# Optimization experiments

Hardware: AMD Instinct MI355X
Metric: run time of the kernel (lower is better)

Reference implementation:

```python
import jax, jax.numpy as jnp
import numpy as np

N_NODES = 50000
N_EDGES = 800000
IN_DIM = 128
HIDDEN = 256
N_CLASSES = 16
N_GRAPHS = 128


def setup_inputs() -> dict:
    key = jax.random.key(0)
    ks = jax.random.split(key, 10)
    x = jax.random.normal(ks[0], (N_NODES, IN_DIM), dtype=jnp.float32)
    edge_index = jax.random.randint(ks[1], (2, N_EDGES), 0, N_NODES, dtype=jnp.int64)
    batch = jnp.sort(jax.random.randint(ks[2], (N_NODES,), 0, N_GRAPHS, dtype=jnp.int64))
    s = 1.0 / np.sqrt(HIDDEN)
    return {
        "x": x,
        "edge_index": edge_index,
        "batch": batch,
        "W_in": jax.random.normal(ks[3], (IN_DIM, HIDDEN), dtype=jnp.float32) / np.sqrt(IN_DIM),
        "b_in": jnp.zeros((HIDDEN,), dtype=jnp.float32),
        "W1": jax.random.normal(ks[4], (HIDDEN, HIDDEN), dtype=jnp.float32) * s,
        "b1": jnp.zeros((HIDDEN,), dtype=jnp.float32),
        "W2": jax.random.normal(ks[5], (HIDDEN, HIDDEN), dtype=jnp.float32) * s,
        "b2": jnp.zeros((HIDDEN,), dtype=jnp.float32),
        "W_out": jax.random.normal(ks[6], (HIDDEN, N_CLASSES), dtype=jnp.float32) * s,
        "b_out": jnp.zeros((N_CLASSES,), dtype=jnp.float32),
    }


def gcn_conv(x, W, b, src, dst):
    # PyG GCNConv: add self-loops, symmetric norm D^-1/2 A D^-1/2, scatter-add at target.
    h = x @ W  # [N, H]
    n = x.shape[0]
    # degree of target nodes, including one self-loop per node
    deg = jax.ops.segment_sum(jnp.ones_like(dst, dtype=h.dtype), dst, num_segments=n) + 1.0
    dinv = deg ** -0.5  # [N]
    norm = dinv[src] * dinv[dst]  # [E]
    msg = h[src] * norm[:, None]  # [E, H]  gather + scale
    agg = jax.ops.segment_sum(msg, dst, num_segments=n)  # scatter-add
    agg = agg + h * (dinv * dinv)[:, None]  # self-loop contribution
    return agg + b


def reference(x, edge_index, batch, W_in, b_in, W1, b1, W2, b2, W_out, b_out):
    src, dst = edge_index[0], edge_index[1]
    h = x @ W_in + b_in
    # layer 1 (dropout is identity in eval mode)
    h = jax.nn.relu(gcn_conv(h, W1, b1, src, dst))
    # layer 2
    h = jax.nn.relu(gcn_conv(h, W2, b2, src, dst))
    # global mean pool over graphs
    sums = jax.ops.segment_sum(h, batch, num_segments=N_GRAPHS)  # [G, H]
    counts = jax.ops.segment_sum(jnp.ones((h.shape[0],), h.dtype), batch, num_segments=N_GRAPHS)
    pooled = sums / jnp.maximum(counts, 1.0)[:, None]
    return pooled @ W_out + b_out  # [G, n_classes]
```

## Files before the change

kernel.cpp:

```cpp
#include <hip/hip_runtime.h>
#include <hip/hip_bf16.h>

typedef __attribute__((ext_vector_type(8))) short bf16x8;
typedef __attribute__((ext_vector_type(4))) float f32x4;

__device__ __forceinline__ unsigned short f2bf(float f) {
    unsigned u = __float_as_uint(f);
    u += 0x7fff + ((u >> 16) & 1);
    return (unsigned short)(u >> 16);
}
__device__ __forceinline__ float bf2f(unsigned short s) {
    return __uint_as_float(((unsigned)s) << 16);
}

#define GL2LDS16(g, l) __builtin_amdgcn_global_load_lds(                      \
        (const __attribute__((address_space(1))) void*)(g),                   \
        (__attribute__((address_space(3))) void*)(l), 16, 0, 0)


__global__ __launch_bounds__(256) void fused_misc_kernel(
        const float* __restrict__ W2, unsigned short* __restrict__ Wt2,
        const float* __restrict__ x, unsigned short* __restrict__ xb, int n4,
        const float* __restrict__ W_in, const float* __restrict__ b_in,
        const float* __restrict__ W1,
        unsigned short* __restrict__ WfT, float* __restrict__ bv,
        const int* __restrict__ src, const int* __restrict__ dst,
        int* __restrict__ cursor, unsigned short* __restrict__ csr16,
        unsigned short* __restrict__ zrow,
        float* __restrict__ sums, int* __restrict__ counts,
        int e, int FB, int WB) {
    __shared__ float row[256];
    __shared__ unsigned short tile[64][65];
    int b = blockIdx.x;
    if (b < FB) {
        int i = b * 256 + threadIdx.x;
        if (i < e) {
            int d = dst[i];
            int p = atomicAdd(&cursor[d], 1);
            if (p < 64) csr16[((size_t)d << 6) + p] = (unsigned short)src[i];
        }
    } else if (b < FB + WB) {
        int k = b - FB;
        int nn = threadIdx.x;
        row[nn] = (k < 128) ? W_in[k * 256 + nn] : b_in[nn];
        __syncthreads();
        float acc = 0.f;
        #pragma unroll 4
        for (int j = 0; j < 256; ++j) acc = fmaf(row[j], W1[j * 256 + nn], acc);
        if (k < 128) WfT[(size_t)nn * 128 + k] = f2bf(acc);
        else bv[nn] = acc;
    } else if (b < FB + WB + 16) {
        int t = b - FB - WB;
        int ti = t >> 2, tj = t & 3;
        int rq = threadIdx.x >> 4;
        int c0 = (threadIdx.x & 15) * 4;
        #pragma unroll
        for (int rr = 0; rr < 64; rr += 16) {
            int r = rr + rq;
            float4 v = *(const float4*)&W2[(size_t)(ti * 64 + r) * 256 + tj * 64 + c0];
            tile[r][c0]     = f2bf(v.x);
            tile[r][c0 + 1] = f2bf(v.y);
            tile[r][c0 + 2] = f2bf(v.z);
            tile[r][c0 + 3] = f2bf(v.w);
        }
        __syncthreads();
        #pragma unroll
        for (int rr = 0; rr < 64; rr += 16) {
            int nrow = rr + rq;
            ushort4 o;
            o.x = tile[c0][nrow];
            o.y = tile[c0 + 1][nrow];
            o.z = tile[c0 + 2][nrow];
            o.w = tile[c0 + 3][nrow];
            *(ushort4*)&Wt2[(size_t)(tj * 64 + nrow) * 256 + ti * 64 + c0] = o;
        }
    } else if (b == FB + WB + 16) {
        if (threadIdx.x < 128) ((unsigned*)zrow)[threadIdx.x] = 0u;
    } else if (b < FB + WB + 16 + 1 + 129) {
        int j = b - (FB + WB + 17);
        if (j < 128) sums[j * 256 + threadIdx.x] = 0.f;
        else if (threadIdx.x < 128) counts[threadIdx.x] = 0;
    } else {
        int i = (b - FB - WB - 17 - 129) * 256 + threadIdx.x;
        if (i < n4) {
            float4 v = ((const float4*)x)[i];
            ushort4 o;
            o.x = f2bf(v.x); o.y = f2bf(v.y); o.z = f2bf(v.z); o.w = f2bf(v.w);
            ((ushort4*)xb)[i] = o;
        }
    }
}


template <int MODE>
__global__ __launch_bounds__(256) void gemm_bf16(const unsigned short* __restrict__ A,
                                                 const unsigned short* __restrict__ Wt,
                                                 const float* __restrict__ aux,
                                                 const float* __restrict__ aux2,
                                                 const float* __restrict__ aux3,
                                                 unsigned short* __restrict__ C,
                                                 int M, int K) {
    __shared__ unsigned short As[128 * 64];
    __shared__ unsigned short Bs[128 * 64];
    const int tid  = threadIdx.x;
    const int lane = tid & 63;
    const int w    = tid >> 6;
    const int wr   = w >> 1, wc = w & 1;
    const int row0 = blockIdx.x * 128;
    const int col0 = blockIdx.y * 128;
    const int mlane = lane & 15, quad = lane >> 4;

    f32x4 acc[4][4];
    #pragma unroll
    for (int i = 0; i < 4; ++i)
        #pragma unroll
        for (int j = 0; j < 4; ++j) acc[i][j] = f32x4{0.f, 0.f, 0.f, 0.f};

    const unsigned short* gA[4]; const unsigned short* gB[4];
    unsigned short* lA[4]; unsigned short* lB[4];
    #pragma unroll
    for (int p = 0; p < 4; ++p) {
        int cid = (p * 4 + w) * 64 + lane;
        int row = cid >> 3, slot = cid & 7;
        int rowA = row0 + row; if (rowA >= M) rowA = M - 1;
        gA[p] = A + (size_t)rowA * K + slot * 8;
        gB[p] = Wt + (size_t)(col0 + row) * K + slot * 8;
        lA[p] = &As[((p * 4 + w) * 64) * 8];
        lB[p] = &Bs[((p * 4 + w) * 64) * 8];
    }

    for (int k0 = 0; k0 < K; k0 += 64) {
        #pragma unroll
        for (int p = 0; p < 4; ++p) GL2LDS16(gA[p] + k0, lA[p]);
        #pragma unroll
        for (int p = 0; p < 4; ++p) GL2LDS16(gB[p] + k0, lB[p]);
        __syncthreads();
        #pragma unroll
        for (int ks = 0; ks < 2; ++ks) {
            bf16x8 af[4], bfv[4];
            #pragma unroll
            for (int i = 0; i < 4; ++i)
                af[i] = *(const bf16x8*)&As[(wr * 64 + i * 16 + mlane) * 64 + ks * 32 + quad * 8];
            #pragma unroll
            for (int j = 0; j < 4; ++j)
                bfv[j] = *(const bf16x8*)&Bs[(wc * 64 + j * 16 + mlane) * 64 + ks * 32 + quad * 8];
            #pragma unroll
            for (int i = 0; i < 4; ++i)
                #pragma unroll
                for (int j = 0; j < 4; ++j)
                    acc[i][j] = __builtin_amdgcn_mfma_f32_16x16x32_bf16(af[i], bfv[j], acc[i][j], 0, 0, 0);
        }
        __syncthreads();
    }

    float bj[4], cj[4];
    if (MODE == 0) {
        #pragma unroll
        for (int j = 0; j < 4; ++j) bj[j] = aux[col0 + wc * 64 + j * 16 + mlane];
    } else if (MODE == 2) {
        #pragma unroll
        for (int j = 0; j < 4; ++j) {
            int gcol = col0 + wc * 64 + j * 16 + mlane;
            bj[j] = aux2[gcol];
            cj[j] = aux3[gcol];
        }
    }
    #pragma unroll
    for (int i = 0; i < 4; ++i) {
        #pragma unroll
        for (int r = 0; r < 4; ++r) {
            int grow = row0 + wr * 64 + i * 16 + quad * 4 + r;
            if (grow < M) {
                float d = 0.f;
                if (MODE == 1) d = rsqrtf((float)((const int*)aux)[grow] + 1.0f);
                else if (MODE == 2) d = aux[grow];
                #pragma unroll
                for (int j = 0; j < 4; ++j) {
                    int gcol = col0 + wc * 64 + j * 16 + mlane;
                    float v = acc[i][j][r];
                    if (MODE == 0)      v = v + bj[j];
                    else if (MODE == 1) v = v * d;
                    else {              v = fmaf(d, bj[j], v) + cj[j]; v = fmaxf(v, 0.f); }
                    C[(size_t)grow * 256 + gcol] = f2bf(v);
                }
            }
        }
    }
}


__global__ __launch_bounds__(256) void agg_x_kernel(const unsigned short* __restrict__ xb,
                                                    const int* __restrict__ deg,
                                                    const unsigned short* __restrict__ csr16,
                                                    unsigned short* __restrict__ ax,
                                                    float* __restrict__ s_out, int n) {
    int node = blockIdx.x * 4 + (threadIdx.x >> 6);
    if (node >= n) return;
    int lane = threadIdx.x & 63;
    int half = lane >> 5, hl = lane & 31;
    const ushort4* x4 = (const ushort4*)xb;
    int cnt = deg[node]; if (cnt > 64) cnt = 64;
    size_t beg = (size_t)node << 6;
    float dn = rsqrtf((float)deg[node] + 1.0f);
    float a0 = 0.f, a1 = 0.f, a2 = 0.f, a3 = 0.f;
    float sdl = 0.f;

    int myi = 0; float mydv = 0.f;
    if (lane < cnt) {
        myi = (int)csr16[beg + lane];
        mydv = rsqrtf((float)deg[myi] + 1.0f);
        sdl += mydv;
    }
    for (int j = 0; j < cnt; j += 8) {
        int s0 = __shfl(myi, j + half),     s1 = __shfl(myi, j + 2 + half);
        int s2 = __shfl(myi, j + 4 + half), s3 = __shfl(myi, j + 6 + half);
        float d0 = __shfl(mydv, j + half),     d1 = __shfl(mydv, j + 2 + half);
        float d2 = __shfl(mydv, j + 4 + half), d3 = __shfl(mydv, j + 6 + half);
        ushort4 v0 = x4[(size_t)s0 * 32 + hl];
        ushort4 v1 = x4[(size_t)s1 * 32 + hl];
        ushort4 v2 = x4[(size_t)s2 * 32 + hl];
        ushort4 v3 = x4[(size_t)s3 * 32 + hl];
        a0 = fmaf(bf2f(v0.x), d0, a0); a1 = fmaf(bf2f(v0.y), d0, a1);
        a2 = fmaf(bf2f(v0.z), d0, a2); a3 = fmaf(bf2f(v0.w), d0, a3);
        a0 = fmaf(bf2f(v1.x), d1, a0); a1 = fmaf(bf2f(v1.y), d1, a1);
        a2 = fmaf(bf2f(v1.z), d1, a2); a3 = fmaf(bf2f(v1.w), d1, a3);
        a0 = fmaf(bf2f(v2.x), d2, a0); a1 = fmaf(bf2f(v2.y), d2, a1);
        a2 = fmaf(bf2f(v2.z), d2, a2); a3 = fmaf(bf2f(v2.w), d2, a3);
        a0 = fmaf(bf2f(v3.x), d3, a0); a1 = fmaf(bf2f(v3.y), d3, a1);
        a2 = fmaf(bf2f(v3.z), d3, a2); a3 = fmaf(bf2f(v3.w), d3, a3);
    }

    a0 += __shfl_xor(a0, 32); a1 += __shfl_xor(a1, 32);
    a2 += __shfl_xor(a2, 32); a3 += __shfl_xor(a3, 32);
    float sd = sdl;
    #pragma unroll
    for (int off = 32; off > 0; off >>= 1) sd += __shfl_down(sd, off);
    if (lane < 32) {
        ushort4 sv = x4[(size_t)node * 32 + hl];
        a0 = fmaf(dn, bf2f(sv.x), a0) * dn;
        a1 = fmaf(dn, bf2f(sv.y), a1) * dn;
        a2 = fmaf(dn, bf2f(sv.z), a2) * dn;
        a3 = fmaf(dn, bf2f(sv.w), a3) * dn;
        ushort4 r;
        r.x = f2bf(a0); r.y = f2bf(a1); r.z = f2bf(a2); r.w = f2bf(a3);
        ((ushort4*)ax)[(size_t)node * 32 + hl] = r;
        if (lane == 0) s_out[node] = dn * (sd + dn);
    }
}


__global__ __launch_bounds__(256) void agg_kernel(const unsigned short* __restrict__ hs,
                                                  const int* __restrict__ deg,
                                                  const unsigned short* __restrict__ csr16,
                                                  const float* __restrict__ bias,
                                                  unsigned short* __restrict__ out, int n) {
    int node = blockIdx.x * 4 + (threadIdx.x >> 6);
    if (node >= n) return;
    int lane = threadIdx.x & 63;
    const ushort4* hs4 = (const ushort4*)hs;
    int cnt = deg[node]; if (cnt > 64) cnt = 64;
    size_t beg = (size_t)node << 6;
    ushort4 sv = hs4[(size_t)node * 64 + lane];
    float a0 = bf2f(sv.x), a1 = bf2f(sv.y), a2 = bf2f(sv.z), a3 = bf2f(sv.w);
    float c0 = 0.f, c1 = 0.f, c2 = 0.f, c3 = 0.f;

    int myi = (lane < cnt) ? (int)csr16[beg + lane] : n;
    for (int j = 0; j < cnt; j += 8) {
        int s0 = __shfl(myi, j + 0), s1 = __shfl(myi, j + 1);
        int s2 = __shfl(myi, j + 2), s3 = __shfl(myi, j + 3);
        int s4 = __shfl(myi, j + 4), s5 = __shfl(myi, j + 5);
        int s6 = __shfl(myi, j + 6), s7 = __shfl(myi, j + 7);
        ushort4 v0 = hs4[(size_t)s0 * 64 + lane];
        ushort4 v1 = hs4[(size_t)s1 * 64 + lane];
        ushort4 v2 = hs4[(size_t)s2 * 64 + lane];
        ushort4 v3 = hs4[(size_t)s3 * 64 + lane];
        ushort4 v4 = hs4[(size_t)s4 * 64 + lane];
        ushort4 v5 = hs4[(size_t)s5 * 64 + lane];
        ushort4 v6 = hs4[(size_t)s6 * 64 + lane];
        ushort4 v7 = hs4[(size_t)s7 * 64 + lane];
        a0 += bf2f(v0.x) + bf2f(v1.x) + bf2f(v2.x) + bf2f(v3.x);
        a1 += bf2f(v0.y) + bf2f(v1.y) + bf2f(v2.y) + bf2f(v3.y);
        a2 += bf2f(v0.z) + bf2f(v1.z) + bf2f(v2.z) + bf2f(v3.z);
        a3 += bf2f(v0.w) + bf2f(v1.w) + bf2f(v2.w) + bf2f(v3.w);
        c0 += bf2f(v4.x) + bf2f(v5.x) + bf2f(v6.x) + bf2f(v7.x);
        c1 += bf2f(v4.y) + bf2f(v5.y) + bf2f(v6.y) + bf2f(v7.y);
        c2 += bf2f(v4.z) + bf2f(v5.z) + bf2f(v6.z) + bf2f(v7.z);
        c3 += bf2f(v4.w) + bf2f(v5.w) + bf2f(v6.w) + bf2f(v7.w);
    }
    a0 += c0; a1 += c1; a2 += c2; a3 += c3;

    float d = rsqrtf((float)deg[node] + 1.0f);
    float4 b = ((const float4*)bias)[lane];
    ushort4 r;
    r.x = f2bf(fmaxf(fmaf(a0, d, b.x), 0.f));
    r.y = f2bf(fmaxf(fmaf(a1, d, b.y), 0.f));
    r.z = f2bf(fmaxf(fmaf(a2, d, b.z), 0.f));
    r.w = f2bf(fmaxf(fmaf(a3, d, b.w), 0.f));
    ((ushort4*)out)[(size_t)node * 64 + lane] = r;
}


__global__ __launch_bounds__(256) void pool_partial_kernel(const unsigned short* __restrict__ h,
                                                           const int* __restrict__ batch,
                                                           float* __restrict__ sums,
                                                           int* __restrict__ counts,
                                                           int n, int chunk) {
    int beg = blockIdx.x * chunk;
    int end = beg + chunk; if (end > n) end = n;
    if (beg >= end) return;
    int c = threadIdx.x;
    int curg = batch[beg];
    float acc = 0.f;
    int runlen = 0;
    for (int i = beg; i < end; ++i) {
        int g = batch[i];
        if (g != curg) {
            atomicAdd(&sums[(size_t)curg * 256 + c], acc);
            if (c == 0) atomicAdd(&counts[curg], runlen);
            acc = 0.f; runlen = 0; curg = g;
        }
        acc += bf2f(h[(size_t)i * 256 + c]);
        ++runlen;
    }
    atomicAdd(&sums[(size_t)curg * 256 + c], acc);
    if (c == 0) atomicAdd(&counts[curg], runlen);
}

__global__ __launch_bounds__(256) void pool_final_kernel(const float* __restrict__ sums,
                                                         const int* __restrict__ counts,
                                                         const float* __restrict__ Wout,
                                                         const float* __restrict__ bout,
                                                         float* __restrict__ out) {
    __shared__ float pl[256];
    int g = blockIdx.x;
    int c = threadIdx.x;
    int cnt = counts[g];
    pl[c] = sums[(size_t)g * 256 + c] / (float)(cnt > 0 ? cnt : 1);
    __syncthreads();
    if (c < 16) {
        float o = bout[c];
        #pragma unroll 4
        for (int k = 0; k < 256; ++k) o = fmaf(pl[k], Wout[k * 16 + c], o);
        out[g * 16 + c] = o;
    }
}


extern "C" void kernel_launch(void* const* d_in, const int* in_sizes, int n_in,
                              void* d_out, int out_size, void* d_ws, size_t ws_size,
                              hipStream_t stream) {
    const float* x     = (const float*)d_in[0];
    const int*   ei    = (const int*)d_in[1];
    const int*   batch = (const int*)d_in[2];
    const float* W_in  = (const float*)d_in[3];
    const float* b_in  = (const float*)d_in[4];
    const float* W1    = (const float*)d_in[5];
    const float* b1    = (const float*)d_in[6];
    const float* W2    = (const float*)d_in[7];
    const float* b2    = (const float*)d_in[8];
    const float* Wout  = (const float*)d_in[9];
    const float* bout  = (const float*)d_in[10];

    const int E = in_sizes[1] / 2;
    const int N = in_sizes[2];
    const int IN_DIM = in_sizes[0] / N;
    const int G = 128;
    const int* src = ei;
    const int* dst = ei + E;

    char* ws = (char*)d_ws;
    size_t off = 0;
    auto alloc = [&](size_t bytes) { size_t p = off; off += (bytes + 255) & ~(size_t)255; return p; };
    unsigned short* bufA = (unsigned short*)(ws + alloc((size_t)N * 256 * 2));
    unsigned short* bufB = (unsigned short*)(ws + alloc((size_t)(N + 1) * 256 * 2));
    unsigned short* xb   = (unsigned short*)(ws + alloc((size_t)N * IN_DIM * 2));
    unsigned short* Wt2  = (unsigned short*)(ws + alloc((size_t)256 * 256 * 2));
    unsigned short* WfT  = (unsigned short*)(ws + alloc((size_t)256 * IN_DIM * 2));
    float*          bv   = (float*)(ws + alloc((size_t)256 * 4));
    float*          sbuf = (float*)(ws + alloc((size_t)N * 4));
    float* sums    = (float*)(ws + alloc((size_t)G * 256 * 4));
    int*   counts  = (int*)(ws + alloc((size_t)G * 4));
    size_t zbeg = off;
    int*   cursor  = (int*)(ws + alloc((size_t)N * 4));
    size_t zend = off;
    unsigned short* csr16 = (unsigned short*)(ws + alloc((size_t)N * 64 * 2));
    (void)ws_size;

    unsigned short* axb = bufB;
    unsigned short* zrow = bufB + (size_t)N * 256;

    const int XB  = (N * IN_DIM / 4 + 255) / 256;
    const int WB  = 129;
    const int FB  = (E + 255) / 256;
    const int SB  = 129;

    hipMemsetAsync(ws + zbeg, 0, zend - zbeg, stream);
    fused_misc_kernel<<<FB + WB + 16 + 1 + SB + XB, 256, 0, stream>>>(
        W2, Wt2, x, xb, N * IN_DIM / 4, W_in, b_in, W1, WfT, bv,
        src, dst, cursor, csr16, zrow, sums, counts, E, FB, WB);

    agg_x_kernel<<<(N + 3) / 4, 256, 0, stream>>>(xb, cursor, csr16, axb, sbuf, N);
    dim3 gg((N + 127) / 128, 2);
    gemm_bf16<2><<<gg, 256, 0, stream>>>(axb, WfT, sbuf, bv, b1, bufA, N, IN_DIM);

    gemm_bf16<1><<<gg, 256, 0, stream>>>(bufA, Wt2, (const float*)cursor, nullptr, nullptr, bufB, N, 256);
    agg_kernel<<<(N + 3) / 4, 256, 0, stream>>>(bufB, cursor, csr16, b2, bufA, N);

    const int PBLOCKS = 512;
    int chunk = (N + PBLOCKS - 1) / PBLOCKS;
    pool_partial_kernel<<<PBLOCKS, 256, 0, stream>>>(bufA, batch, sums, counts, N, chunk);
    pool_final_kernel<<<G, 256, 0, stream>>>(sums, counts, Wout, bout, (float*)d_out);
}
```

Before: 329.4 us.

## Widen GEMM tile to full 256 columns with 512-thread blocks

Each GEMM block now covers all 256 output columns for a 128-row tile, using 8 waves (2x4) instead of 4, with A and B staged together in one shared buffer. Before, two column blocks each reloaded the same A tile, so this removes that duplicate A traffic and halves the grid. In exchange each block needs more LDS and registers, which can lower occupancy, and there are fewer blocks to spread across CUs.

New measurement: 315.1 us, median of 2. -4.4%, faster.

```diff
diff --git a/kernel.cpp b/kernel.cpp
--- a/kernel.cpp
+++ b/kernel.cpp
@@ -93,21 +93,19 @@
 
 
 template <int MODE>
-__global__ __launch_bounds__(256) void gemm_bf16(const unsigned short* __restrict__ A,
+__global__ __launch_bounds__(512) void gemm_bf16(const unsigned short* __restrict__ A,
                                                  const unsigned short* __restrict__ Wt,
                                                  const float* __restrict__ aux,
                                                  const float* __restrict__ aux2,
                                                  const float* __restrict__ aux3,
                                                  unsigned short* __restrict__ C,
                                                  int M, int K) {
-    __shared__ unsigned short As[128 * 64];
-    __shared__ unsigned short Bs[128 * 64];
+    __shared__ unsigned short S[3072 * 8];
     const int tid  = threadIdx.x;
     const int lane = tid & 63;
     const int w    = tid >> 6;
-    const int wr   = w >> 1, wc = w & 1;
+    const int wr   = w >> 2, wc = w & 3;
     const int row0 = blockIdx.x * 128;
-    const int col0 = blockIdx.y * 128;
     const int mlane = lane & 15, quad = lane >> 4;
 
     f32x4 acc[4][4];
@@ -116,34 +114,35 @@
         #pragma unroll
         for (int j = 0; j < 4; ++j) acc[i][j] = f32x4{0.f, 0.f, 0.f, 0.f};
 
-    const unsigned short* gA[4]; const unsigned short* gB[4];
-    unsigned short* lA[4]; unsigned short* lB[4];
+    const unsigned short* g[6]; unsigned short* l[6];
     #pragma unroll
-    for (int p = 0; p < 4; ++p) {
-        int cid = (p * 4 + w) * 64 + lane;
-        int row = cid >> 3, slot = cid & 7;
-        int rowA = row0 + row; if (rowA >= M) rowA = M - 1;
-        gA[p] = A + (size_t)rowA * K + slot * 8;
-        gB[p] = Wt + (size_t)(col0 + row) * K + slot * 8;
-        lA[p] = &As[((p * 4 + w) * 64) * 8];
-        lB[p] = &Bs[((p * 4 + w) * 64) * 8];
+    for (int q = 0; q < 6; ++q) {
+        int cid = q * 512 + tid;
+        l[q] = &S[(q * 512 + w * 64) * 8];
+        if (cid < 1024) {
+            int r = cid >> 3, slot = cid & 7;
+            int rowA = row0 + r; if (rowA >= M) rowA = M - 1;
+            g[q] = A + (size_t)rowA * K + slot * 8;
+        } else {
+            int j = cid - 1024;
+            int col = j >> 3, slot = j & 7;
+            g[q] = Wt + (size_t)col * K + slot * 8;
+        }
     }
 
     for (int k0 = 0; k0 < K; k0 += 64) {
         #pragma unroll
-        for (int p = 0; p < 4; ++p) GL2LDS16(gA[p] + k0, lA[p]);
-        #pragma unroll
-        for (int p = 0; p < 4; ++p) GL2LDS16(gB[p] + k0, lB[p]);
+        for (int q = 0; q < 6; ++q) GL2LDS16(g[q] + k0, l[q]);
         __syncthreads();
         #pragma unroll
         for (int ks = 0; ks < 2; ++ks) {
             bf16x8 af[4], bfv[4];
             #pragma unroll
             for (int i = 0; i < 4; ++i)
-                af[i] = *(const bf16x8*)&As[(wr * 64 + i * 16 + mlane) * 64 + ks * 32 + quad * 8];
+                af[i] = *(const bf16x8*)&S[(wr * 64 + i * 16 + mlane) * 64 + ks * 32 + quad * 8];
             #pragma unroll
             for (int j = 0; j < 4; ++j)
-                bfv[j] = *(const bf16x8*)&Bs[(wc * 64 + j * 16 + mlane) * 64 + ks * 32 + quad * 8];
+                bfv[j] = *(const bf16x8*)&S[8192 + (wc * 64 + j * 16 + mlane) * 64 + ks * 32 + quad * 8];
             #pragma unroll
             for (int i = 0; i < 4; ++i)
                 #pragma unroll
@@ -156,11 +155,11 @@
     float bj[4], cj[4];
     if (MODE == 0) {
         #pragma unroll
-        for (int j = 0; j < 4; ++j) bj[j] = aux[col0 + wc * 64 + j * 16 + mlane];
+        for (int j = 0; j < 4; ++j) bj[j] = aux[wc * 64 + j * 16 + mlane];
     } else if (MODE == 2) {
         #pragma unroll
         for (int j = 0; j < 4; ++j) {
-            int gcol = col0 + wc * 64 + j * 16 + mlane;
+            int gcol = wc * 64 + j * 16 + mlane;
             bj[j] = aux2[gcol];
             cj[j] = aux3[gcol];
         }
@@ -176,7 +175,7 @@
                 else if (MODE == 2) d = aux[grow];
                 #pragma unroll
                 for (int j = 0; j < 4; ++j) {
-                    int gcol = col0 + wc * 64 + j * 16 + mlane;
+                    int gcol = wc * 64 + j * 16 + mlane;
                     float v = acc[i][j][r];
                     if (MODE == 0)      v = v + bj[j];
                     else if (MODE == 1) v = v * d;
@@ -393,6 +392,7 @@
     const int WB  = 129;
     const int FB  = (E + 255) / 256;
     const int SB  = 129;
+    const int MB  = (N + 127) / 128;
 
     hipMemsetAsync(ws + zbeg, 0, zend - zbeg, stream);
     fused_misc_kernel<<<FB + WB + 16 + 1 + SB + XB, 256, 0, stream>>>(
@@ -400,10 +400,9 @@
         src, dst, cursor, csr16, zrow, sums, counts, E, FB, WB);
 
     agg_x_kernel<<<(N + 3) / 4, 256, 0, stream>>>(xb, cursor, csr16, axb, sbuf, N);
-    dim3 gg((N + 127) / 128, 2);
-    gemm_bf16<2><<<gg, 256, 0, stream>>>(axb, WfT, sbuf, bv, b1, bufA, N, IN_DIM);
-
-    gemm_bf16<1><<<gg, 256, 0, stream>>>(bufA, Wt2, (const float*)cursor, nullptr, nullptr, bufB, N, 256);
+    gemm_bf16<2><<<MB, 512, 0, stream>>>(axb, WfT, sbuf, bv, b1, bufA, N, IN_DIM);
+
+    gemm_bf16<1><<<MB, 512, 0, stream>>>(bufA, Wt2, (const float*)cursor, nullptr, nullptr, bufB, N, 256);
     agg_kernel<<<(N + 3) / 4, 256, 0, stream>>>(bufB, cursor, csr16, b2, bufA, N);
 
     const int PBLOCKS = 512;
```
